# Kernel tuning notes

Hardware: AMD Instinct MI355X
Metric: run time of the kernel (lower is better)

## Reference

```python
import jax, jax.numpy as jnp
import numpy as np

NODES_PER_GRAPH = 40
NEG_SLOPE = 0.1


def gcn_conv(x, src, dst, deg_inv_sqrt, W, b):
    # PyG GCNConv: h = x @ W.T; symmetric-normalized aggregation with self-loops; + bias
    h = x @ W.T                                   # [N, out]
    norm = deg_inv_sqrt[src] * deg_inv_sqrt[dst]  # [E]
    msgs = h[src] * norm[:, None]                 # [E, out]
    agg = jax.ops.segment_sum(msgs, dst, num_segments=x.shape[0])
    # self-loop contribution: norm_ii = deg_inv_sqrt[i]^2 = 1/deg[i]
    agg = agg + h * (deg_inv_sqrt ** 2)[:, None]
    return agg + b


def setup_inputs() -> dict:
    key = jax.random.key(0)
    ks = jax.random.split(key, 12)
    N, E, C = 200000, 1000000, 40
    hid1, hid2, hid3, lin1, lin2, out = 128, 256, 128, 512, 128, 1

    def glorot(k, shape):
        fan_in = shape[-1]
        return jax.random.normal(k, shape, dtype=jnp.float32) * (1.0 / np.sqrt(fan_in))

    x = jax.random.normal(ks[0], (N, C), dtype=jnp.float32)
    edge_index = jax.random.randint(ks[1], (2, E), 0, N, dtype=jnp.int64)
    return {
        "x": x,
        "edge_index": edge_index,
        "W1": glorot(ks[2], (hid1, C)), "b1": jnp.zeros((hid1,), jnp.float32),
        "W2": glorot(ks[3], (hid2, hid1)), "b2": jnp.zeros((hid2,), jnp.float32),
        "W3": glorot(ks[4], (hid3, hid2)), "b3": jnp.zeros((hid3,), jnp.float32),
        "L1w": glorot(ks[5], (lin1, NODES_PER_GRAPH * hid3)), "L1b": jnp.zeros((lin1,), jnp.float32),
        "L2w": glorot(ks[6], (lin2, lin1)), "L2b": jnp.zeros((lin2,), jnp.float32),
        "L3w": glorot(ks[7], (out, lin2)), "L3b": jnp.zeros((out,), jnp.float32),
    }


def reference(x, edge_index, W1, b1, W2, b2, W3, b3, L1w, L1b, L2w, L2b, L3w, L3b):
    N = x.shape[0]
    src, dst = edge_index[0], edge_index[1]
    # degree with self-loops (edge weight 1), shared by all three convs
    deg = jax.ops.segment_sum(jnp.ones_like(dst, dtype=x.dtype), dst, num_segments=N) + 1.0
    deg_inv_sqrt = jax.lax.rsqrt(deg)

    lrelu = lambda v: jax.nn.leaky_relu(v, NEG_SLOPE)

    h = lrelu(gcn_conv(x, src, dst, deg_inv_sqrt, W1, b1))
    # dropout is identity in eval mode
    h = lrelu(gcn_conv(h, src, dst, deg_inv_sqrt, W2, b2))
    h = lrelu(gcn_conv(h, src, dst, deg_inv_sqrt, W3, b3))

    g = h.reshape(N // NODES_PER_GRAPH, -1)   # [G, 40*hid3]
    g = lrelu(g @ L1w.T + L1b)
    g = lrelu(g @ L2w.T + L2b)
    g = g @ L3w.T + L3b
    return jax.nn.sigmoid(g)                   # [G, 1]
```

## Files before the change

kernel.cpp:

```cpp
#include <hip/hip_runtime.h>
#include <cmath>

#define CDIV(a,b) (((a)+(b)-1)/(b))

typedef unsigned short bf16_t;
using short8 = __attribute__((ext_vector_type(8))) short;
using f32x4  = __attribute__((ext_vector_type(4))) float;
using u16x4  = __attribute__((ext_vector_type(4))) unsigned short;
using u16x8  = __attribute__((ext_vector_type(8))) unsigned short;

__device__ __forceinline__ float bf2f(unsigned short b) {
    unsigned u = ((unsigned)b) << 16;
    float f;
    __builtin_memcpy(&f, &u, 4);
    return f;
}
__device__ __forceinline__ unsigned short f2bf(float f) {
    unsigned u;
    __builtin_memcpy(&u, &f, 4);
    u = (u + 0x7FFFu + ((u >> 16) & 1u)) >> 16;
    return (unsigned short)u;
}

__device__ __forceinline__ void gload16(const bf16_t* g, unsigned short* l) {
    __builtin_amdgcn_global_load_lds(
        (const __attribute__((address_space(1))) void*)(g),
        (__attribute__((address_space(3))) void*)(l), 16, 0, 0);
}

__device__ __forceinline__ int edge_src(const int* ei, int E, int f, int i) {
    return f ? ei[2 * (size_t)i] : ei[i];
}
__device__ __forceinline__ int edge_dst(const int* ei, int E, int f, int i) {
    return f ? ei[2 * ((size_t)E + (size_t)i)] : ei[(size_t)E + (size_t)i];
}

__global__ __launch_bounds__(256) void k_packhist(const int* __restrict__ ei, int E,
                                                  int* __restrict__ src32,
                                                  int* __restrict__ dst32,
                                                  int* __restrict__ cnt8, int N) {
    __shared__ int sflag;
    int t = threadIdx.x;
    if (t < 64) {
        unsigned v = (unsigned)ei[2 * t + 1];
        unsigned long long m = __ballot(v != 0u);
        if (t == 0) sflag = (m == 0ULL) ? 1 : 0;
    }
    __syncthreads();
    int i = blockIdx.x * 256 + t;
    if (i >= E) return;
    int f = sflag;
    int s = edge_src(ei, E, f, i);
    int d = edge_dst(ei, E, f, i);
    src32[i] = s;
    dst32[i] = d;
    if ((unsigned)d < (unsigned)N)
        atomicAdd(&cnt8[(blockIdx.x & 7) * N + d], 1);
}

__global__ void k_blockred(const int* __restrict__ cnt8, int* __restrict__ bsum, int N) {
    __shared__ int sd[256];
    int b = blockIdx.x, t = threadIdx.x;
    int base = b * 1024 + t * 4;
    int s = 0;
#pragma unroll
    for (int i = 0; i < 4; i++) {
        int idx = base + i;
        if (idx < N)
#pragma unroll
            for (int r = 0; r < 8; r++) s += cnt8[r * N + idx];
    }
    sd[t] = s; __syncthreads();
    for (int off = 128; off > 0; off >>= 1) { if (t < off) sd[t] += sd[t + off]; __syncthreads(); }
    if (t == 0) bsum[b] = sd[0];
}

__global__ void k_scanwrite(const int* __restrict__ cnt8, const int* __restrict__ bsum,
                            int* __restrict__ rowptr, int* __restrict__ cur,
                            float* __restrict__ dis, int N, int nb) {
    __shared__ int sb[256];
    __shared__ int sd[256];
    int b = blockIdx.x, t = threadIdx.x;
    int v0 = (t < nb) ? bsum[t] : 0;
    sb[t] = v0; __syncthreads();
    for (int off = 1; off < 256; off <<= 1) {
        int y = (t >= off) ? sb[t - off] : 0;
        __syncthreads();
        sb[t] += y;
        __syncthreads();
    }
    int block_pre = (b == 0) ? 0 : sb[b - 1];

    int base = b * 1024 + t * 4;
    int tot[4]; int s = 0;
#pragma unroll
    for (int i = 0; i < 4; i++) {
        int idx = base + i;
        tot[i] = 0;
        if (idx < N) {
#pragma unroll
            for (int r = 0; r < 8; r++) tot[i] += cnt8[r * N + idx];
        }
        s += tot[i];
    }
    sd[t] = s; __syncthreads();
    for (int off = 1; off < 256; off <<= 1) {
        int y = (t >= off) ? sd[t - off] : 0;
        __syncthreads();
        sd[t] += y;
        __syncthreads();
    }
    int pre = block_pre + sd[t] - s;
#pragma unroll
    for (int i = 0; i < 4; i++) {
        int idx = base + i;
        if (idx < N) {
            rowptr[idx] = pre;
            cur[idx] = pre;
            dis[idx] = rsqrtf((float)tot[i] + 1.0f);
            pre += tot[i];
        } else if (idx == N) {
            rowptr[N] = pre;
        }
    }
}

#define FILL_EPB 4096
__global__ __launch_bounds__(256) void k_fill_r(
        const int* __restrict__ src32, const int* __restrict__ dst32, int E,
        int* __restrict__ cur, int* __restrict__ csr, int N, int NR) {
    int r = blockIdx.x & 7;
    int chunk = blockIdx.x >> 3;
    int lo = r * NR;
    int hi = min(lo + NR, N);
    int base = chunk * FILL_EPB;
    int end = min(base + FILL_EPB, E);
    for (int i = base + threadIdx.x; i < end; i += 256) {
        int d = dst32[i];
        if (d >= lo && d < hi) {
            int s = src32[i];
            if ((unsigned)s < (unsigned)N) {
                int p = atomicAdd(&cur[d], 1);
                csr[p] = s;
            }
        }
    }
}


struct WcSeg { const float* src; bf16_t* dst; int M, KW, KP, nchunk; };

__global__ __launch_bounds__(256) void k_wconv(WcSeg s0, WcSeg s1, WcSeg s2,
                                               WcSeg s3, WcSeg s4, WcSeg s5,
                                               int wtotal, int* __restrict__ zdst,
                                               int total) {
    int i = blockIdx.x * 256 + threadIdx.x;
    if (i >= total) return;
    if (i >= wtotal) {
        int4 z = {0, 0, 0, 0};
        *(int4*)(zdst + (size_t)(i - wtotal) * 4) = z;
        return;
    }
    WcSeg s;
    if (i < s0.nchunk) s = s0;
    else if ((i -= s0.nchunk) < s1.nchunk) s = s1;
    else if ((i -= s1.nchunk) < s2.nchunk) s = s2;
    else if ((i -= s2.nchunk) < s3.nchunk) s = s3;
    else if ((i -= s3.nchunk) < s4.nchunk) s = s4;
    else { i -= s4.nchunk; s = s5; }
    int cpr = s.KP >> 3;
    int row = i / cpr, kk = (i % cpr) << 3;
    short8 v = {};
    if (kk < s.KW) {
        const float4* p = (const float4*)(s.src + (size_t)row * s.KW + kk);
        float4 a = p[0], b = p[1];
        v[0] = (short)f2bf(a.x); v[1] = (short)f2bf(a.y);
        v[2] = (short)f2bf(a.z); v[3] = (short)f2bf(a.w);
        v[4] = (short)f2bf(b.x); v[5] = (short)f2bf(b.y);
        v[6] = (short)f2bf(b.z); v[7] = (short)f2bf(b.w);
    }
    *(short8*)(s.dst + (size_t)row * s.KP + kk) = v;
}


template <bool CBF, bool BIAS, int ACT, bool SPLIT, bool SCALE>
__global__ __launch_bounds__(256) void gemm_mfma(
        const bf16_t* __restrict__ A, const bf16_t* __restrict__ Wb,
        const float* __restrict__ bias, void* __restrict__ Cv,
        int N, int K, int M, int Kseg, int nx, int ny,
        const float* __restrict__ rowscale) {
    constexpr int BM = 128, BK = 64;
    __shared__ __align__(16) unsigned short lds[4 * 64 * 68];
    unsigned short* Als = lds;
    unsigned short* Bls = lds + BM * BK;

    int t = threadIdx.x;
    int lane = t & 63, wid = t >> 6;
    int quad = lane >> 4, l15 = lane & 15;
    int wave_m = wid & 1, wave_n = wid >> 1;

    int bx, by, bz;
    if (SPLIT) {
        int bid = (int)blockIdx.x;
        int xcd = bid & 7, li = bid >> 3;
        bx = li % nx;
        int pl = li / nx;
        int ppx = (int)(gridDim.x >> 3) / nx;
        int pair = xcd * ppx + pl;
        by = pair % ny;
        bz = pair / ny;
    } else {
        bx = blockIdx.x; by = blockIdx.y; bz = 0;
    }

    int bm0 = by * BM;
    int bn0 = bx * BM;
    int kbeg = SPLIT ? bz * Kseg : 0;
    int kend = SPLIT ? min(kbeg + Kseg, K) : K;

    f32x4 acc[4][4] = {};

    for (int k0 = kbeg; k0 < kend; k0 += BK) {
#pragma unroll
        for (int it = 0; it < 4; it++) {
            int idx = t + it * 256;
            int row = idx >> 3, sc = idx & 7;
            int c = sc ^ (row & 7);
            int ga = bm0 + row; if (ga >= N) ga = N - 1;
            gload16(A + (size_t)ga * K + k0 + c * 8, Als + idx * 8);
            gload16(Wb + (size_t)(bn0 + row) * K + k0 + c * 8, Bls + idx * 8);
        }
        __syncthreads();

#pragma unroll
        for (int ks = 0; ks < 2; ks++) {
            short8 af[4], bfr[4];
            int ck = ks * 4 + quad;
            int sw = (ck ^ (l15 & 7)) << 3;
#pragma unroll
            for (int mt = 0; mt < 4; mt++)
                af[mt] = *(const short8*)&Als[(wave_m * 64 + mt * 16 + l15) * BK + sw];
#pragma unroll
            for (int nt = 0; nt < 4; nt++)
                bfr[nt] = *(const short8*)&Bls[(wave_n * 64 + nt * 16 + l15) * BK + sw];
#pragma unroll
            for (int mt = 0; mt < 4; mt++)
#pragma unroll
                for (int nt = 0; nt < 4; nt++)
                    acc[mt][nt] = __builtin_amdgcn_mfma_f32_16x16x32_bf16(
                        af[mt], bfr[nt], acc[mt][nt], 0, 0, 0);
        }
        __syncthreads();
    }

    if (!SPLIT && CBF) {
        constexpr int TST = 68;
        unsigned short* tw = lds + wid * 64 * TST;
#pragma unroll
        for (int mt = 0; mt < 4; mt++) {
#pragma unroll
            for (int nt = 0; nt < 4; nt++) {
                int tcol = nt * 16 + l15;
                float bv = BIAS ? bias[bn0 + wave_n * 64 + tcol] : 0.f;
#pragma unroll
                for (int r = 0; r < 4; r++) {
                    float x = acc[mt][nt][r];
                    if (BIAS) x += bv;
                    if (ACT == 1) x = x > 0.f ? x : 0.1f * x;
                    if (SCALE) {
                        int row = bm0 + wave_m * 64 + mt * 16 + quad * 4 + r;
                        x *= rowscale[row < N ? row : N - 1];
                    }
                    tw[(mt * 16 + quad * 4 + r) * TST + tcol] = f2bf(x);
                }
            }
        }
        __syncthreads();
        bf16_t* C = (bf16_t*)Cv;
        int lrow0 = lane >> 3, lcol = (lane & 7) * 8;
#pragma unroll
        for (int it = 0; it < 8; it++) {
            int lrow = it * 8 + lrow0;
            int row = bm0 + wave_m * 64 + lrow;
            if (row < N) {
                u16x8 v = *(const u16x8*)&tw[lrow * TST + lcol];
                *(u16x8*)&C[(size_t)row * M + bn0 + wave_n * 64 + lcol] = v;
            }
        }
    } else {
        float* Pz = SPLIT ? ((float*)Cv + (size_t)bz * N * M) : (float*)Cv;
#pragma unroll
        for (int mt = 0; mt < 4; mt++) {
            int rbase = bm0 + wave_m * 64 + mt * 16 + quad * 4;
#pragma unroll
            for (int nt = 0; nt < 4; nt++) {
                int col = bn0 + wave_n * 64 + nt * 16 + l15;
                float bv = (BIAS && !SPLIT) ? bias[col] : 0.f;
#pragma unroll
                for (int r = 0; r < 4; r++) {
                    int row = rbase + r;
                    if (row >= N) continue;
                    float x = acc[mt][nt][r];
                    if (!SPLIT) {
                        if (BIAS) x += bv;
                        if (ACT == 1) x = x > 0.f ? x : 0.1f * x;
                    }
                    Pz[(size_t)row * M + col] = x;
                }
            }
        }
    }
}

__global__ __launch_bounds__(256) void gemm_mlp2(
        const float* __restrict__ part6,
        const float* __restrict__ L1b,
        const bf16_t* __restrict__ Wb,
        float* __restrict__ Pout,
        int G) {
    constexpr int BM = 128, BK = 64, K = 512, M = 128, NY = 40;
    __shared__ __align__(16) unsigned short lds[2 * BM * BK];
    unsigned short* Als = lds;
    unsigned short* Bls = lds + BM * BK;

    int t = threadIdx.x;
    int lane = t & 63, wid = t >> 6;
    int quad = lane >> 4, l15 = lane & 15;
    int wave_m = wid & 1, wave_n = wid >> 1;

    int bid = (int)blockIdx.x;
    int xcd = bid & 7, li = bid >> 3;
    int ppx = (int)(gridDim.x >> 3);
    int pair = xcd * ppx + li;
    int by = pair % NY;
    int bz = pair / NY;

    int bm0 = by * BM;
    int kbeg = bz * (K / 4);
    size_t GK = (size_t)G * K;

    f32x4 acc[4][4] = {};

    for (int k0 = kbeg; k0 < kbeg + K / 4; k0 += BK) {
#pragma unroll
        for (int it = 0; it < 4; it++) {
            int idx = t + it * 256;
            int row = idx >> 3, sc = idx & 7;
            int cW = sc ^ (row & 7);
            gload16(Wb + (size_t)row * K + k0 + cW * 8, Bls + idx * 8);
            int g = bm0 + row; if (g >= G) g = G - 1;
            const float* pb = part6 + (size_t)g * K + k0 + sc * 8;
            float v[8] = {};
#pragma unroll
            for (int z = 0; z < 6; z++) {
                const float* pz = pb + (size_t)z * GK;
                float4 a = *(const float4*)pz;
                float4 b = *(const float4*)(pz + 4);
                v[0] += a.x; v[1] += a.y; v[2] += a.z; v[3] += a.w;
                v[4] += b.x; v[5] += b.y; v[6] += b.z; v[7] += b.w;
            }
            float4 b0 = *(const float4*)&L1b[k0 + sc * 8];
            float4 b1 = *(const float4*)&L1b[k0 + sc * 8 + 4];
            float bb[8] = {b0.x, b0.y, b0.z, b0.w, b1.x, b1.y, b1.z, b1.w};
            u16x8 o;
#pragma unroll
            for (int j = 0; j < 8; j++) {
                float xv = v[j] + bb[j];
                xv = xv > 0.f ? xv : 0.1f * xv;
                o[j] = f2bf(xv);
            }
            *(u16x8*)&Als[row * BK + ((sc ^ (row & 7)) << 3)] = o;
        }
        __syncthreads();

#pragma unroll
        for (int ks = 0; ks < 2; ks++) {
            short8 af[4], bfr[4];
            int ck = ks * 4 + quad;
            int sw = (ck ^ (l15 & 7)) << 3;
#pragma unroll
            for (int mt = 0; mt < 4; mt++)
                af[mt] = *(const short8*)&Als[(wave_m * 64 + mt * 16 + l15) * BK + sw];
#pragma unroll
            for (int nt = 0; nt < 4; nt++)
                bfr[nt] = *(const short8*)&Bls[(wave_n * 64 + nt * 16 + l15) * BK + sw];
#pragma unroll
            for (int mt = 0; mt < 4; mt++)
#pragma unroll
                for (int nt = 0; nt < 4; nt++)
                    acc[mt][nt] = __builtin_amdgcn_mfma_f32_16x16x32_bf16(
                        af[mt], bfr[nt], acc[mt][nt], 0, 0, 0);
        }
        __syncthreads();
    }

    float* Pz = Pout + (size_t)bz * G * M;
#pragma unroll
    for (int mt = 0; mt < 4; mt++) {
        int rbase = bm0 + wave_m * 64 + mt * 16 + quad * 4;
#pragma unroll
        for (int nt = 0; nt < 4; nt++) {
            int col = wave_n * 64 + nt * 16 + l15;
#pragma unroll
            for (int r = 0; r < 4; r++) {
                int row = rbase + r;
                if (row >= G) continue;
                Pz[(size_t)row * M + col] = acc[mt][nt][r];
            }
        }
    }
}

__global__ __launch_bounds__(256, 3) void gemm_fused23(
        const bf16_t* __restrict__ H1,
        const int* __restrict__ rowptr, const int* __restrict__ csr,
        const float* __restrict__ dis,
        const bf16_t* __restrict__ W2,
        const float*  __restrict__ b2,
        const bf16_t* __restrict__ W3,
        bf16_t* __restrict__ C,
        int N) {
    __shared__ __align__(16) unsigned short lds[24576];
    unsigned short* Als  = lds;
    unsigned short* Bls  = lds + 8192;
    unsigned short* H2ls = lds;
    unsigned short* B2ls = lds + 16384;

    int t = threadIdx.x;
    int lane = t & 63, wid = t >> 6;
    int quad = lane >> 4, l15 = lane & 15;
    int wm = wid & 1, wn = wid >> 1;
    int bm0 = blockIdx.x * 64;

    float bv[8];
#pragma unroll
    for (int nt = 0; nt < 8; nt++) bv[nt] = b2[wn * 128 + nt * 16 + l15];

#pragma unroll
    for (int it = 0; it < 8; it++) {
        int idx = t + it * 256;
        int row = idx >> 3, sc = idx & 7;
        int c = sc ^ (row & 7);
        gload16(W2 + (size_t)row * 128 + c * 8, Bls + idx * 8);
    }

    {
        int r = t >> 2, l4 = t & 3;
        int row = bm0 + r; if (row >= N) row = N - 1;
        int cb = l4 * 32;
        const bf16_t* Hrow = H1 + (size_t)row * 128 + cb;
        float acc[32];
        {
            u16x8 v[4];
#pragma unroll
            for (int j = 0; j < 4; j++) v[j] = *(const u16x8*)(Hrow + j * 8);
#pragma unroll
            for (int j = 0; j < 4; j++)
#pragma unroll
                for (int f = 0; f < 8; f++) acc[j * 8 + f] = bf2f(v[j][f]);
        }
        int s = rowptr[row], e = rowptr[row + 1];
        int p = s;
        for (; p + 4 <= e; p += 4) {
            int s0 = csr[p], s1 = csr[p + 1], s2 = csr[p + 2], s3 = csr[p + 3];
            const bf16_t* p0 = H1 + (size_t)s0 * 128 + cb;
            const bf16_t* p1 = H1 + (size_t)s1 * 128 + cb;
            const bf16_t* p2 = H1 + (size_t)s2 * 128 + cb;
            const bf16_t* p3 = H1 + (size_t)s3 * 128 + cb;
            u16x8 a0[4], a1[4], a2[4], a3[4];
#pragma unroll
            for (int j = 0; j < 4; j++) {
                a0[j] = *(const u16x8*)(p0 + j * 8);
                a1[j] = *(const u16x8*)(p1 + j * 8);
                a2[j] = *(const u16x8*)(p2 + j * 8);
                a3[j] = *(const u16x8*)(p3 + j * 8);
            }
#pragma unroll
            for (int j = 0; j < 4; j++)
#pragma unroll
                for (int f = 0; f < 8; f++)
                    acc[j * 8 + f] += (bf2f(a0[j][f]) + bf2f(a1[j][f]))
                                    + (bf2f(a2[j][f]) + bf2f(a3[j][f]));
        }
        if (p + 2 <= e) {
            int s0 = csr[p], s1 = csr[p + 1];
            const bf16_t* p0 = H1 + (size_t)s0 * 128 + cb;
            const bf16_t* p1 = H1 + (size_t)s1 * 128 + cb;
            u16x8 a0[4], a1[4];
#pragma unroll
            for (int j = 0; j < 4; j++) { a0[j] = *(const u16x8*)(p0 + j * 8);
                                          a1[j] = *(const u16x8*)(p1 + j * 8); }
#pragma unroll
            for (int j = 0; j < 4; j++)
#pragma unroll
                for (int f = 0; f < 8; f++)
                    acc[j * 8 + f] += bf2f(a0[j][f]) + bf2f(a1[j][f]);
            p += 2;
        }
        if (p < e) {
            int s0 = csr[p];
            const bf16_t* p0 = H1 + (size_t)s0 * 128 + cb;
            u16x8 a0[4];
#pragma unroll
            for (int j = 0; j < 4; j++) a0[j] = *(const u16x8*)(p0 + j * 8);
#pragma unroll
            for (int j = 0; j < 4; j++)
#pragma unroll
                for (int f = 0; f < 8; f++) acc[j * 8 + f] += bf2f(a0[j][f]);
        }
        float di = dis[row];
#pragma unroll
        for (int j = 0; j < 4; j++) {
            int col0 = cb + j * 8;
            int h = col0 >> 6;
            int ck = (col0 & 63) >> 3;
            int swc = ck ^ (r & 7);
            u16x8 o;
#pragma unroll
            for (int f = 0; f < 8; f++) o[f] = f2bf(acc[j * 8 + f] * di);
            *(u16x8*)&Als[h * 4096 + r * 64 + (swc << 3)] = o;
        }
    }
    __syncthreads();

    f32x4 acc1[2][8] = {};
    for (int h = 0; h < 2; h++) {
        if (h > 0) {
#pragma unroll
            for (int it = 0; it < 8; it++) {
                int idx = t + it * 256;
                int row = idx >> 3, sc = idx & 7;
                int c = sc ^ (row & 7);
                gload16(W2 + (size_t)row * 128 + 64 + c * 8, Bls + idx * 8);
            }
            __syncthreads();
        }
#pragma unroll
        for (int ks = 0; ks < 2; ks++) {
            int ck = ks * 4 + quad;
            int sw = (ck ^ (l15 & 7)) << 3;
            short8 af[2];
#pragma unroll
            for (int mt = 0; mt < 2; mt++)
                af[mt] = *(const short8*)&Als[h * 4096 + (wm * 32 + mt * 16 + l15) * 64 + sw];
#pragma unroll
            for (int nt = 0; nt < 8; nt++) {
                short8 bfr = *(const short8*)&Bls[(wn * 128 + nt * 16 + l15) * 64 + sw];
#pragma unroll
                for (int mt = 0; mt < 2; mt++)
                    acc1[mt][nt] = __builtin_amdgcn_mfma_f32_16x16x32_bf16(
                        af[mt], bfr, acc1[mt][nt], 0, 0, 0);
            }
        }
        __syncthreads();
    }

#pragma unroll
    for (int it = 0; it < 4; it++) {
        int idx = t + it * 256;
        int row = idx >> 3, sc = idx & 7;
        int c = sc ^ (row & 7);
        gload16(W3 + (size_t)row * 256 + c * 8, B2ls + idx * 8);
    }

#pragma unroll
    for (int mt = 0; mt < 2; mt++) {
#pragma unroll
        for (int nt = 0; nt < 8; nt++) {
            int col = wn * 128 + nt * 16 + l15;
            int chunk = col >> 3, within = col & 7;
#pragma unroll
            for (int r = 0; r < 4; r++) {
                int row = wm * 32 + mt * 16 + quad * 4 + r;
                float xv = acc1[mt][nt][r] + bv[nt];
                xv = xv > 0.f ? xv : 0.1f * xv;
                H2ls[row * 256 + ((chunk ^ (row & 7)) << 3) + within] = f2bf(xv);
            }
        }
    }
    __syncthreads();

    f32x4 acc2[2][4] = {};
    for (int k0 = 0; k0 < 256; k0 += 64) {
        if (k0 > 0) {
#pragma unroll
            for (int it = 0; it < 4; it++) {
                int idx = t + it * 256;
                int row = idx >> 3, sc = idx & 7;
                int c = sc ^ (row & 7);
                gload16(W3 + (size_t)row * 256 + k0 + c * 8, B2ls + idx * 8);
            }
            __syncthreads();
        }
#pragma unroll
        for (int ks = 0; ks < 2; ks++) {
            int kc = (k0 >> 3) + ks * 4 + quad;
            int swa = (kc ^ (l15 & 7)) << 3;
            int swb = ((ks * 4 + quad) ^ (l15 & 7)) << 3;
            short8 af[2], bfr[4];
#pragma unroll
            for (int mt = 0; mt < 2; mt++)
                af[mt] = *(const short8*)&H2ls[(wm * 32 + mt * 16 + l15) * 256 + swa];
#pragma unroll
            for (int nt = 0; nt < 4; nt++)
                bfr[nt] = *(const short8*)&B2ls[(wn * 64 + nt * 16 + l15) * 64 + swb];
#pragma unroll
            for (int mt = 0; mt < 2; mt++)
#pragma unroll
                for (int nt = 0; nt < 4; nt++)
                    acc2[mt][nt] = __builtin_amdgcn_mfma_f32_16x16x32_bf16(
                        af[mt], bfr[nt], acc2[mt][nt], 0, 0, 0);
        }
        __syncthreads();
    }

    constexpr int TST = 68;
    unsigned short* tw = lds + wid * 32 * TST;
#pragma unroll
    for (int mt = 0; mt < 2; mt++) {
#pragma unroll
        for (int r = 0; r < 4; r++) {
            int row = bm0 + wm * 32 + mt * 16 + quad * 4 + r;
            float ds = dis[row < N ? row : N - 1];
#pragma unroll
            for (int nt = 0; nt < 4; nt++) {
                int tcol = nt * 16 + l15;
                tw[(mt * 16 + quad * 4 + r) * TST + tcol] = f2bf(acc2[mt][nt][r] * ds);
            }
        }
    }
    __syncthreads();
    int lrow0 = lane >> 3, lcol = (lane & 7) * 8;
#pragma unroll
    for (int it = 0; it < 4; it++) {
        int lrow = it * 8 + lrow0;
        int row = bm0 + wm * 32 + lrow;
        if (row < N) {
            u16x8 v = *(const u16x8*)&tw[lrow * TST + lcol];
            *(u16x8*)&C[(size_t)row * 128 + wn * 64 + lcol] = v;
        }
    }
}


template <int F, bool BACT, bool PRE>
__global__ __launch_bounds__(256) void k_agg(
        const bf16_t* __restrict__ H, const int* __restrict__ rowptr,
        const int* __restrict__ csr, const float* __restrict__ dis,
        const float* __restrict__ bias, bf16_t* __restrict__ out, int N) {
    constexpr int SUB = F / 8;
    constexpr int NPW = 64 / SUB;
    constexpr int SH  = (SUB == 16) ? 4 : 3;
    int gtid = blockIdx.x * 256 + threadIdx.x;
    int wave = gtid >> 6, lane = gtid & 63;
    int sub = lane >> SH, sl = lane & (SUB - 1);
    int node = wave * NPW + sub;
    if (node >= N) return;
    float di = dis[node];
    int s = rowptr[node], e = rowptr[node + 1];

    auto load_row = [&](const bf16_t* p, float (&r)[8]) {
        u16x8 v = *(const u16x8*)p;
#pragma unroll
        for (int f = 0; f < 8; f++) r[f] = bf2f(v[f]);
    };

    float acc[8], acc2[8];
    {
        float r[8];
        load_row(H + (size_t)node * F + sl * 8, r);
        float sln = PRE ? 1.f : di * di;
#pragma unroll
        for (int f = 0; f < 8; f++) { acc[f] = r[f] * sln; acc2[f] = 0.f; }
    }
    int p = s;
    for (; p + 4 <= e; p += 4) {
        int s0 = csr[p], s1 = csr[p + 1], s2 = csr[p + 2], s3 = csr[p + 3];
        float r0[8], r1[8], r2[8], r3[8];
        load_row(H + (size_t)s0 * F + sl * 8, r0);
        load_row(H + (size_t)s1 * F + sl * 8, r1);
        load_row(H + (size_t)s2 * F + sl * 8, r2);
        load_row(H + (size_t)s3 * F + sl * 8, r3);
        if (PRE) {
#pragma unroll
            for (int f = 0; f < 8; f++) {
                acc[f]  += r0[f] + r2[f];
                acc2[f] += r1[f] + r3[f];
            }
        } else {
            float n0 = dis[s0] * di, n1 = dis[s1] * di;
            float n2 = dis[s2] * di, n3 = dis[s3] * di;
#pragma unroll
            for (int f = 0; f < 8; f++) {
                acc[f]  += r0[f] * n0; acc2[f] += r1[f] * n1;
                acc[f]  += r2[f] * n2; acc2[f] += r3[f] * n3;
            }
        }
    }
    if (p + 2 <= e) {
        int s0 = csr[p], s1 = csr[p + 1];
        float r0[8], r1[8];
        load_row(H + (size_t)s0 * F + sl * 8, r0);
        load_row(H + (size_t)s1 * F + sl * 8, r1);
        if (PRE) {
#pragma unroll
            for (int f = 0; f < 8; f++) { acc[f] += r0[f]; acc2[f] += r1[f]; }
        } else {
            float n0 = dis[s0] * di, n1 = dis[s1] * di;
#pragma unroll
            for (int f = 0; f < 8; f++) { acc[f] += r0[f] * n0; acc2[f] += r1[f] * n1; }
        }
        p += 2;
    }
    if (p < e) {
        int s0 = csr[p];
        float r0[8];
        load_row(H + (size_t)s0 * F + sl * 8, r0);
        if (PRE) {
#pragma unroll
            for (int f = 0; f < 8; f++) acc[f] += r0[f];
        } else {
            float n0 = dis[s0] * di;
#pragma unroll
            for (int f = 0; f < 8; f++) acc[f] += r0[f] * n0;
        }
    }

    float o[8];
#pragma unroll
    for (int f = 0; f < 8; f++) {
        float v = acc[f] + acc2[f];
        if (PRE) v *= di;
        if (BACT) {
            v += bias[sl * 8 + f];
            v = v > 0.f ? v : 0.1f * v;
        }
        o[f] = v;
    }
    u16x8 w = {f2bf(o[0]), f2bf(o[1]), f2bf(o[2]), f2bf(o[3]),
               f2bf(o[4]), f2bf(o[5]), f2bf(o[6]), f2bf(o[7])};
    *(u16x8*)(out + (size_t)node * F + sl * 8) = w;
}


__global__ __launch_bounds__(256) void k_head2(
        const float* __restrict__ part, const float* __restrict__ L2b,
        const float* __restrict__ L3w, const float* __restrict__ L3b,
        float* __restrict__ out, int G) {
    int wv = (int)((blockIdx.x * blockDim.x + threadIdx.x) >> 6);
    int lane = threadIdx.x & 63;
    if (wv >= G) return;
    size_t base = (size_t)wv * 128 + lane * 2;
    size_t GM = (size_t)G * 128;
    float2 s = *(const float2*)&part[base];
#pragma unroll
    for (int z = 1; z < 4; z++) {
        float2 p = *(const float2*)&part[z * GM + base];
        s.x += p.x; s.y += p.y;
    }
    float2 b = *(const float2*)&L2b[lane * 2];
    float vx = s.x + b.x, vy = s.y + b.y;
    vx = vx > 0.f ? vx : 0.1f * vx;
    vy = vy > 0.f ? vy : 0.1f * vy;
    float2 wl = *(const float2*)&L3w[lane * 2];
    float d = vx * wl.x + vy * wl.y;
    for (int off = 32; off > 0; off >>= 1) d += __shfl_xor(d, off, 64);
    if (lane == 0) out[wv] = 1.f / (1.f + expf(-(d + L3b[0])));
}


extern "C" void kernel_launch(void* const* d_in, const int* in_sizes, int n_in,
                              void* d_out, int out_size, void* d_ws, size_t ws_size,
                              hipStream_t stream) {
    const float* x   = (const float*)d_in[0];
    const int*   ei  = (const int*)d_in[1];
    const float* W1  = (const float*)d_in[2];  const float* b1  = (const float*)d_in[3];
    const float* W2  = (const float*)d_in[4];  const float* b2  = (const float*)d_in[5];
    const float* W3  = (const float*)d_in[6];  const float* b3  = (const float*)d_in[7];
    const float* L1w = (const float*)d_in[8];  const float* L1b = (const float*)d_in[9];
    const float* L2w = (const float*)d_in[10]; const float* L2b = (const float*)d_in[11];
    const float* L3w = (const float*)d_in[12]; const float* L3b = (const float*)d_in[13];
    float* out = (float*)d_out;

    const int C = 40;
    const int N = in_sizes[0] / C;
    const int E = in_sizes[1] / 2;
    const int G = N / 40;
    const int H1d = 128, H2d = 256, H3d = 128, M1 = 512, M2 = 128;
    const int K1 = 40 * H3d;

    char* wsb = (char*)d_ws;
    size_t off = 0;
    auto alloc = [&](size_t bytes) -> void* {
        void* p = wsb + off;
        off += (bytes + 255) & ~(size_t)255;
        return p;
    };
    int*    cnt8   = (int*)alloc(4 * 8 * (size_t)N);
    int*    rowptr = (int*)alloc(4 * (size_t)(N + 1));
    int*    cur    = (int*)alloc(4 * (size_t)N);
    int*    csr    = (int*)alloc(4 * (size_t)E);
    int*    bsum   = (int*)alloc(4 * 512);
    float*  dis    = (float*)alloc(4 * (size_t)N);
    bf16_t* Hb     = (bf16_t*)alloc(2 * (size_t)N * H2d);
    bf16_t* Xb     = (bf16_t*)alloc(2 * (size_t)N * H2d);
    bf16_t* W1b    = (bf16_t*)alloc(2 * (size_t)H1d * 64);
    bf16_t* W2b    = (bf16_t*)alloc(2 * (size_t)H2d * H1d);
    bf16_t* W3b    = (bf16_t*)alloc(2 * (size_t)H3d * H2d);
    bf16_t* L1wb   = (bf16_t*)alloc(2 * (size_t)M1 * K1);
    bf16_t* L2wb   = (bf16_t*)alloc(2 * (size_t)M2 * M1);
    if (off > ws_size) return;

    int* src32 = (int*)Xb;
    int* dst32 = src32 + E;
    bf16_t* xb   = Hb;
    bf16_t* A1b  = Xb;
    bf16_t* H1   = Hb;
    bf16_t* H3p  = Xb;
    bf16_t* X3   = Hb;
    float*  part = (float*)Xb;
    float*  part2 = part + 6 * (size_t)G * M1;

    WcSeg s0 = {W1,  W1b,  H1d, 40,  64,  H1d * 64 / 8};
    WcSeg s1 = {W2,  W2b,  H2d, H1d, H1d, H2d * H1d / 8};
    WcSeg s2 = {W3,  W3b,  H3d, H2d, H2d, H3d * H2d / 8};
    WcSeg s3 = {L1w, L1wb, M1,  K1,  K1,  M1 * K1 / 8};
    WcSeg s4 = {L2w, L2wb, M2,  M1,  M1,  M2 * M1 / 8};
    WcSeg s5 = {x,   xb,   N,   40,  64,  N * 64 / 8};
    int wtotal = s0.nchunk + s1.nchunk + s2.nchunk + s3.nchunk + s4.nchunk + s5.nchunk;
    int ztotal = wtotal + 2 * N;
    k_wconv<<<CDIV(ztotal, 256), 256, 0, stream>>>(s0, s1, s2, s3, s4, s5,
                                                   wtotal, cnt8, ztotal);

    k_packhist<<<CDIV(E, 256), 256, 0, stream>>>(ei, E, src32, dst32, cnt8, N);
    int nb = CDIV(N + 1, 1024);
    k_blockred<<<nb, 256, 0, stream>>>(cnt8, bsum, N);
    k_scanwrite<<<nb, 256, 0, stream>>>(cnt8, bsum, rowptr, cur, dis, N, nb);
    int NR = CDIV(N, 8);
    k_fill_r<<<8 * CDIV(E, FILL_EPB), 256, 0, stream>>>(src32, dst32, E, cur, csr, N, NR);

    const int NB = CDIV(N, 128);

    k_agg<64, false, false><<<CDIV(N, 32), 256, 0, stream>>>(xb, rowptr, csr, dis, nullptr, A1b, N);
    gemm_mfma<true, true, 1, false, true><<<dim3(1, NB), 256, 0, stream>>>(A1b, W1b, b1, H1, N, 64, H1d, 0, 0, 0, dis);
    gemm_fused23<<<CDIV(N, 64), 256, 0, stream>>>(H1, rowptr, csr, dis, W2b, b2, W3b, H3p, N);
    k_agg<128, true, true><<<CDIV(N, 16), 256, 0, stream>>>(H3p, rowptr, csr, dis, b3, X3, N);

    gemm_mfma<false, false, 0, true, false><<<960, 256, 0, stream>>>(X3, L1wb, nullptr, part, G, K1, M1, 896, 4, 40, nullptr);
    gemm_mlp2<<<160, 256, 0, stream>>>(part, L1b, L2wb, part2, G);
    k_head2<<<CDIV(G, 4), 256, 0, stream>>>(part2, L2b, L3w, L3b, out, G);
}
```

Before: 456.8 us.

## Fuse layer-1 neighbor aggregation into the layer-1 MFMA GEMM kernel

Replaces the separate layer-1 aggregation kernel and the GEMM with one kernel. Each block gathers normalized neighbor features for 128 rows straight into LDS, then runs the 64x128 MFMA with bias, leaky-relu and the dis scaling, and writes H1 through an LDS transpose. This removes the round trip of the aggregated A1 buffer through global memory and one launch. In exchange, the gather now uses only 2 threads per row, so parallelism during the latency-bound gather phase is lower. Buffer aliases are swapped to fit the new dataflow.

```diff
diff --git a/kernel.cpp b/kernel.cpp
--- a/kernel.cpp
+++ b/kernel.cpp
@@ -308,6 +308,141 @@
                     Pz[(size_t)row * M + col] = x;
                 }
             }
+        }
+    }
+}
+
+__global__ __launch_bounds__(256, 4) void gemm_fused1(
+        const bf16_t* __restrict__ xb,
+        const int* __restrict__ rowptr, const int* __restrict__ csr,
+        const float* __restrict__ dis,
+        const bf16_t* __restrict__ W1,
+        const float* __restrict__ b1,
+        bf16_t* __restrict__ H1,
+        int N) {
+    __shared__ __align__(16) unsigned short lds[17408];
+    unsigned short* Als = lds;
+    unsigned short* Bls = lds + 8192;
+
+    int t = threadIdx.x;
+    int lane = t & 63, wid = t >> 6;
+    int quad = lane >> 4, l15 = lane & 15;
+    int wave_m = wid & 1, wave_n = wid >> 1;
+    int bm0 = blockIdx.x * 128;
+
+#pragma unroll
+    for (int it = 0; it < 4; it++) {
+        int idx = t + it * 256;
+        int row = idx >> 3, sc = idx & 7;
+        int c = sc ^ (row & 7);
+        gload16(W1 + (size_t)row * 64 + c * 8, Bls + idx * 8);
+    }
+
+    {
+        int r = t >> 1, l2 = t & 1;
+        int row = bm0 + r; if (row >= N) row = N - 1;
+        int cb = l2 * 32;
+        const bf16_t* Xrow = xb + (size_t)row * 64 + cb;
+        float di = dis[row];
+        float acc[32];
+        {
+            u16x8 v[4];
+#pragma unroll
+            for (int j = 0; j < 4; j++) v[j] = *(const u16x8*)(Xrow + j * 8);
+            float sln = di * di;
+#pragma unroll
+            for (int j = 0; j < 4; j++)
+#pragma unroll
+                for (int f = 0; f < 8; f++) acc[j * 8 + f] = bf2f(v[j][f]) * sln;
+        }
+        int s = rowptr[row], e = rowptr[row + 1];
+        int p = s;
+        for (; p + 2 <= e; p += 2) {
+            int s0 = csr[p], s1 = csr[p + 1];
+            float n0 = dis[s0] * di, n1 = dis[s1] * di;
+            const bf16_t* p0 = xb + (size_t)s0 * 64 + cb;
+            const bf16_t* p1 = xb + (size_t)s1 * 64 + cb;
+            u16x8 a0[4], a1[4];
+#pragma unroll
+            for (int j = 0; j < 4; j++) { a0[j] = *(const u16x8*)(p0 + j * 8);
+                                          a1[j] = *(const u16x8*)(p1 + j * 8); }
+#pragma unroll
+            for (int j = 0; j < 4; j++)
+#pragma unroll
+                for (int f = 0; f < 8; f++)
+                    acc[j * 8 + f] += bf2f(a0[j][f]) * n0 + bf2f(a1[j][f]) * n1;
+        }
+        if (p < e) {
+            int s0 = csr[p];
+            float n0 = dis[s0] * di;
+            const bf16_t* p0 = xb + (size_t)s0 * 64 + cb;
+            u16x8 a0[4];
+#pragma unroll
+            for (int j = 0; j < 4; j++) a0[j] = *(const u16x8*)(p0 + j * 8);
+#pragma unroll
+            for (int j = 0; j < 4; j++)
+#pragma unroll
+                for (int f = 0; f < 8; f++) acc[j * 8 + f] += bf2f(a0[j][f]) * n0;
+        }
+#pragma unroll
+        for (int j = 0; j < 4; j++) {
+            int ck = l2 * 4 + j;
+            int swc = ck ^ (r & 7);
+            u16x8 o;
+#pragma unroll
+            for (int f = 0; f < 8; f++) o[f] = f2bf(acc[j * 8 + f]);
+            *(u16x8*)&Als[r * 64 + (swc << 3)] = o;
+        }
+    }
+    __syncthreads();
+
+    f32x4 acc[4][4] = {};
+#pragma unroll
+    for (int ks = 0; ks < 2; ks++) {
+        short8 af[4], bfr[4];
+        int ck = ks * 4 + quad;
+        int sw = (ck ^ (l15 & 7)) << 3;
+#pragma unroll
+        for (int mt = 0; mt < 4; mt++)
+            af[mt] = *(const short8*)&Als[(wave_m * 64 + mt * 16 + l15) * 64 + sw];
+#pragma unroll
+        for (int nt = 0; nt < 4; nt++)
+            bfr[nt] = *(const short8*)&Bls[(wave_n * 64 + nt * 16 + l15) * 64 + sw];
+#pragma unroll
+        for (int mt = 0; mt < 4; mt++)
+#pragma unroll
+            for (int nt = 0; nt < 4; nt++)
+                acc[mt][nt] = __builtin_amdgcn_mfma_f32_16x16x32_bf16(
+                    af[mt], bfr[nt], acc[mt][nt], 0, 0, 0);
+    }
+    __syncthreads();
+
+    constexpr int TST = 68;
+    unsigned short* tw = lds + wid * 64 * TST;
+#pragma unroll
+    for (int mt = 0; mt < 4; mt++) {
+#pragma unroll
+        for (int r = 0; r < 4; r++) {
+            int row = bm0 + wave_m * 64 + mt * 16 + quad * 4 + r;
+            float ds = dis[row < N ? row : N - 1];
+#pragma unroll
+            for (int nt = 0; nt < 4; nt++) {
+                int tcol = nt * 16 + l15;
+                float x = acc[mt][nt][r] + b1[wave_n * 64 + tcol];
+                x = x > 0.f ? x : 0.1f * x;
+                tw[(mt * 16 + quad * 4 + r) * TST + tcol] = f2bf(x * ds);
+            }
+        }
+    }
+    __syncthreads();
+    int lrow0 = lane >> 3, lcol = (lane & 7) * 8;
+#pragma unroll
+    for (int it = 0; it < 8; it++) {
+        int lrow = it * 8 + lrow0;
+        int row = bm0 + wave_m * 64 + lrow;
+        if (row < N) {
+            u16x8 v = *(const u16x8*)&tw[lrow * TST + lcol];
+            *(u16x8*)&H1[(size_t)row * 128 + wave_n * 64 + lcol] = v;
         }
     }
 }
@@ -814,11 +949,10 @@
     int* src32 = (int*)Xb;
     int* dst32 = src32 + E;
     bf16_t* xb   = Hb;
-    bf16_t* A1b  = Xb;
-    bf16_t* H1   = Hb;
-    bf16_t* H3p  = Xb;
-    bf16_t* X3   = Hb;
-    float*  part = (float*)Xb;
+    bf16_t* H1   = Xb;
+    bf16_t* H3p  = Hb;
+    bf16_t* X3   = Xb;
+    float*  part = (float*)Hb;
     float*  part2 = part + 6 * (size_t)G * M1;
 
     WcSeg s0 = {W1,  W1b,  H1d, 40,  64,  H1d * 64 / 8};
@@ -839,10 +973,7 @@
     int NR = CDIV(N, 8);
     k_fill_r<<<8 * CDIV(E, FILL_EPB), 256, 0, stream>>>(src32, dst32, E, cur, csr, N, NR);
 
-    const int NB = CDIV(N, 128);
-
-    k_agg<64, false, false><<<CDIV(N, 32), 256, 0, stream>>>(xb, rowptr, csr, dis, nullptr, A1b, N);
-    gemm_mfma<true, true, 1, false, true><<<dim3(1, NB), 256, 0, stream>>>(A1b, W1b, b1, H1, N, 64, H1d, 0, 0, 0, dis);
+    gemm_fused1<<<CDIV(N, 128), 256, 0, stream>>>(xb, rowptr, csr, dis, W1b, b1, H1, N);
     gemm_fused23<<<CDIV(N, 64), 256, 0, stream>>>(H1, rowptr, csr, dis, W2b, b2, W3b, H3p, N);
     k_agg<128, true, true><<<CDIV(N, 16), 256, 0, stream>>>(H3p, rowptr, csr, dis, b3, X3, N);
 
```

New measurement: 446.4 us. -2.3%, faster.
